# Kernel optimization log

Measured on AMD Instinct MI355X. Metric: run time of the kernel, lower is better.

Reference implementation:

```python
import jax, jax.numpy as jnp
import numpy as np
import math

B_CAPS, C_CAPS, K, P, STRIDE, ITERS = 32, 32, 3, 4, 2, 3
PSIZE = P * P
EPS = 1e-8
LAMBDA = 1e-3
LN_2PI = math.log(2.0 * math.pi)


def setup_inputs() -> dict:
    key = jax.random.key(0)
    k1, k2 = jax.random.split(key)
    # input: (b, h, w, B*(P*P+1)); activations must be non-negative (sigmoid-range)
    x = jax.random.uniform(k1, (4, 16, 16, B_CAPS * (PSIZE + 1)), dtype=jnp.float32)
    # nn.Parameter(torch.randn(1, K*K*B, P, P))
    weights = jax.random.normal(k2, (1, K * K * B_CAPS, P, P), dtype=jnp.float32)
    beta_u = jnp.zeros((C_CAPS,), jnp.float32)
    beta_a = jnp.zeros((C_CAPS,), jnp.float32)
    return {"x": x, "weights": weights, "beta_u": beta_u, "beta_a": beta_a}


def _add_patches(x):
    # torch add_pathes: zero-pad 1 on each side, gather KxK patches with stride
    b, h, w, c = x.shape
    x = jnp.pad(x, ((0, 0), (1, 1), (1, 1), (0, 0)))
    hp = h + 2
    oh = (hp - K) // STRIDE + 1
    idxs = np.arange(0, hp - K + 1, STRIDE)[:, None] + np.arange(K)[None, :]  # (oh, K)
    x = x[:, idxs, :, :]        # (b, oh, K, hp, c)
    x = x[:, :, :, idxs, :]     # (b, oh, K, ow, K, c)
    x = jnp.transpose(x, (0, 1, 3, 2, 4, 5))  # (b, oh, ow, K, K, c)
    return x, oh, oh


def _m_step(a_in, r, v, beta_u, beta_a):
    # a_in: (n, Bk, 1), r: (n, Bk, C), v: (n, Bk, C, psize)
    n = v.shape[0]
    r = r * a_in
    r = r / (jnp.sum(r, axis=2, keepdims=True) + EPS)
    r_sum = jnp.sum(r, axis=1, keepdims=True)              # (n, 1, C)
    coeff = (r / (r_sum + EPS))[..., None]                 # (n, Bk, C, 1)
    mu = jnp.sum(coeff * v, axis=1, keepdims=True)         # (n, 1, C, psize)
    sigma_sq = jnp.sum(coeff * (v - mu) ** 2, axis=1, keepdims=True) + EPS
    # cost_h: (n, C, psize)
    cost_h = (beta_u[:, None] + jnp.log(jnp.sqrt(sigma_sq[:, 0]))) * jnp.transpose(r_sum, (0, 2, 1))
    a_out = jax.nn.sigmoid(LAMBDA * (beta_a - jnp.sum(cost_h, axis=2)))  # (n, C)
    return a_out, mu, sigma_sq


def _e_step(mu, sigma_sq, a_out, v):
    ln_p = -(v - mu) ** 2 / (2.0 * sigma_sq) - jnp.log(jnp.sqrt(sigma_sq)) - 0.5 * LN_2PI
    ln_ap = jnp.sum(ln_p, axis=3) + jnp.log(a_out)[:, None, :]  # (n, Bk, C)
    return jax.nn.softmax(ln_ap, axis=2)


def _em_routing(v, a_in, beta_u, beta_a):
    n, Bk, C, _ = v.shape
    r = jnp.full((n, Bk, C), 1.0 / C, dtype=v.dtype)
    mu = a_out = None
    for it in range(ITERS):
        a_out, mu, sigma_sq = _m_step(a_in, r, v, beta_u, beta_a)
        if it < ITERS - 1:
            r = _e_step(mu, sigma_sq, a_out, v)
    return mu, a_out


def reference(x, weights, beta_u, beta_a):
    b = x.shape[0]
    patches, oh, ow = _add_patches(x)                       # (b, oh, ow, K, K, B*(psize+1))
    n = b * oh * ow
    Bk = K * K * B_CAPS
    p_in = patches[..., : B_CAPS * PSIZE].reshape(n, Bk, P, P)
    a_in = patches[..., B_CAPS * PSIZE :].reshape(n, Bk, 1)
    # votes: pose_i @ W_i (weights have no C axis in this repo -> shared across out-caps)
    v = jnp.einsum("nipq,iqr->nipr", p_in, weights[0]).reshape(n, Bk, 1, PSIZE)
    v = jnp.broadcast_to(v, (n, Bk, C_CAPS, PSIZE))
    mu, a_out = _em_routing(v, a_in, beta_u, beta_a)
    p_out = mu.reshape(b, oh, ow, C_CAPS * PSIZE)
    a_out = a_out.reshape(b, oh, ow, C_CAPS)
    return jnp.concatenate([p_out, a_out], axis=-1)        # (b, oh, ow, C*(psize+1))
```

## Files before the change

### kernel.cpp

```cpp
#include <hip/hip_runtime.h>
#include <math.h>

#define NTH 1024

typedef unsigned uint2v __attribute__((ext_vector_type(2)));

template <int CTRL>
__device__ __forceinline__ float dpp_mov(float x) {
  return __int_as_float(__builtin_amdgcn_mov_dpp(__float_as_int(x), CTRL, 0xF, 0xF, true));
}
__device__ __forceinline__ float row_sum16(float x) {
  x += dpp_mov<0x128>(x);
  x += dpp_mov<0x124>(x);
  x += dpp_mov<0x122>(x);
  x += dpp_mov<0x121>(x);
  return x;
}
__device__ __forceinline__ float row_max16(float x) {
  x = fmaxf(x, dpp_mov<0x128>(x));
  x = fmaxf(x, dpp_mov<0x124>(x));
  x = fmaxf(x, dpp_mov<0x122>(x));
  x = fmaxf(x, dpp_mov<0x121>(x));
  return x;
}
__device__ __forceinline__ float sum32(float x) {
  x = row_sum16(x);
  uint2v p = __builtin_amdgcn_permlane16_swap(__float_as_uint(x), __float_as_uint(x), false, false);
  return __uint_as_float(p.x) + __uint_as_float(p.y);
}
__device__ __forceinline__ float max32(float x) {
  x = row_max16(x);
  uint2v p = __builtin_amdgcn_permlane16_swap(__float_as_uint(x), __float_as_uint(x), false, false);
  return fmaxf(__uint_as_float(p.x), __uint_as_float(p.y));
}
__device__ __forceinline__ float sum_halves(float x) {
  uint2v p = __builtin_amdgcn_permlane32_swap(__float_as_uint(x), __float_as_uint(x), false, false);
  return __uint_as_float(p.x) + __uint_as_float(p.y);
}

__device__ __forceinline__ int swz8(int q, int c) { return (q + c) & 7; }

__launch_bounds__(NTH, 4)
__global__ void convcaps_em_kernel(const float* __restrict__ x,
                                   const float* __restrict__ wts,
                                   const float* __restrict__ beta_u,
                                   const float* __restrict__ beta_a,
                                   float* __restrict__ out) {
  constexpr int BK = 288;
  constexpr float EPS = 1e-8f;
  constexpr float LAM = 1e-3f;

  __shared__ __align__(16) float v_lds[BK * 16];
  __shared__ float w_lds[BK];
  __shared__ __align__(8) float part_lds[32 * 32];
  __shared__ float rsum_lds[32];
  __shared__ __align__(16) float stage_lds[16 * 1024];
  __shared__ __align__(16) float muinv2_lds[32 * 32];
  __shared__ float lnac_lds[32];
  __shared__ float mu0_lds[16], i2s0_lds[16], sc0_lds[2];

  const int t = threadIdx.x;
  const int n = blockIdx.x;
  const int b  = n >> 6;
  const int oy = (n >> 3) & 7;
  const int ox = n & 7;

  if (t < BK) {
    const int kk = t >> 5, cap = t & 31;
    const int kh = kk / 3, kw = kk - kh * 3;
    const int iy = oy * 2 - 1 + kh, ix = ox * 2 - 1 + kw;
    float val = 0.0f;
    if ((unsigned)iy < 16u && (unsigned)ix < 16u)
      val = x[(((b * 16 + iy) * 16) + ix) * 544 + 512 + cap];
    w_lds[t] = val / (val + EPS);
  }
  for (int task = t; task < BK * 4; task += NTH) {
    const int i = task >> 2, p = task & 3;
    const int kk = i >> 5, cap = i & 31;
    const int kh = kk / 3, kw = kk - kh * 3;
    const int iy = oy * 2 - 1 + kh, ix = ox * 2 - 1 + kw;
    float4 vv = make_float4(0.f, 0.f, 0.f, 0.f);
    if ((unsigned)iy < 16u && (unsigned)ix < 16u) {
      const float* px = x + ((((b * 16 + iy) * 16) + ix) * 544 + cap * 16 + p * 4);
      const float4 pin = *reinterpret_cast<const float4*>(px);
      const float* pw = wts + i * 16;
      const float4 w0 = *reinterpret_cast<const float4*>(pw + 0);
      const float4 w1 = *reinterpret_cast<const float4*>(pw + 4);
      const float4 w2 = *reinterpret_cast<const float4*>(pw + 8);
      const float4 w3 = *reinterpret_cast<const float4*>(pw + 12);
      vv.x = pin.x * w0.x + pin.y * w1.x + pin.z * w2.x + pin.w * w3.x;
      vv.y = pin.x * w0.y + pin.y * w1.y + pin.z * w2.y + pin.w * w3.y;
      vv.z = pin.x * w0.z + pin.y * w1.z + pin.z * w2.z + pin.w * w3.z;
      vv.w = pin.x * w0.w + pin.y * w1.w + pin.z * w2.w + pin.w * w3.w;
    }
    *reinterpret_cast<float4*>(&v_lds[i * 16 + p * 4]) = vv;
  }
  __syncthreads();

  const int c32 = t & 31;
  const int g32 = t >> 5;
  const int wv  = t >> 6;
  const int ln  = t & 63;
  const int cS  = (t >> 4) & 31;
  const int pS  = t & 15;
  const float bu = beta_u[cS];
  const float ba = beta_a[cS];

  if (t < 512) {
    const int h = t >> 4;
    float aw = 0.f, a1 = 0.f, a2 = 0.f;
    #pragma unroll
    for (int k = 0; k < 9; ++k) {
      const int i = h * 9 + k;
      const float wvv = w_lds[i];
      const float vv = v_lds[i * 16 + pS];
      aw += wvv;
      a1 = fmaf(wvv, vv, a1);
      a2 = fmaf(wvv * vv, vv, a2);
    }
    *reinterpret_cast<float2*>(&part_lds[(h * 16 + pS) * 2]) = make_float2(a1, a2);
    if (pS == 0) rsum_lds[h] = aw;
  }
  __syncthreads();
  if (t < 16) {
    float m0 = 0.f, a1 = 0.f, a2 = 0.f;
    #pragma unroll
    for (int h = 0; h < 32; ++h) {
      m0 += rsum_lds[h];
      const float2 f2 = *reinterpret_cast<const float2*>(&part_lds[(h * 16 + t) * 2]);
      a1 += f2.x; a2 += f2.y;
    }
    const float D0 = m0 + 32.f * EPS;
    const float mu = a1 / D0;
    float sig = (a2 - mu * (2.f * a1 - mu * m0)) / D0;
    sig = fmaxf(sig, 0.f) + EPS;
    const float ls = row_sum16(0.5f * __logf(sig));
    mu0_lds[t] = mu;
    i2s0_lds[t] = 0.5f / sig;
    if (t == 0) { sc0_lds[0] = m0 * 0.03125f; sc0_lds[1] = ls; }
  }
  __syncthreads();
  if (t < 512) {
    *reinterpret_cast<float2*>(
        &muinv2_lds[cS * 32 + (swz8(pS >> 1, cS) << 2) + ((pS & 1) << 1)]) =
        make_float2(mu0_lds[pS], i2s0_lds[pS]);
    if (pS == 0) {
      const float rs0 = sc0_lds[0], ls = sc0_lds[1];
      const float z = LAM * (ba - rs0 * (16.f * bu + ls));
      lnac_lds[cS] = -__logf(1.f + __expf(-z)) - ls;
    }
  }
  __syncthreads();

  for (int it = 0; it < 2; ++it) {
    {
      float muc[16], isc[16];
      #pragma unroll
      for (int q = 0; q < 8; ++q) {
        const float4 f =
            *reinterpret_cast<const float4*>(&muinv2_lds[c32 * 32 + (swz8(q, c32) << 2)]);
        muc[2 * q] = f.x; isc[2 * q] = f.y;
        muc[2 * q + 1] = f.z; isc[2 * q + 1] = f.w;
      }
      const float lna = lnac_lds[c32];
      const float lmax = max32(lna);
      float s1[16], s2[16];
      #pragma unroll
      for (int p2 = 0; p2 < 16; ++p2) { s1[p2] = 0.f; s2[p2] = 0.f; }
      float colsum = 0.f;
      #pragma unroll 3
      for (int pass = 0; pass < 9; ++pass) {
        const int i = pass * 32 + g32;
        const float4 v0 = *reinterpret_cast<const float4*>(&v_lds[i * 16 + 0]);
        const float4 v1 = *reinterpret_cast<const float4*>(&v_lds[i * 16 + 4]);
        const float4 v2 = *reinterpret_cast<const float4*>(&v_lds[i * 16 + 8]);
        const float4 v3 = *reinterpret_cast<const float4*>(&v_lds[i * 16 + 12]);
        float a0 = 0.f, a1 = 0.f, a2 = 0.f, a3 = 0.f, d;
        d = v0.x - muc[0];  a0 = fmaf(d * d, isc[0],  a0);
        d = v0.y - muc[1];  a1 = fmaf(d * d, isc[1],  a1);
        d = v0.z - muc[2];  a2 = fmaf(d * d, isc[2],  a2);
        d = v0.w - muc[3];  a3 = fmaf(d * d, isc[3],  a3);
        d = v1.x - muc[4];  a0 = fmaf(d * d, isc[4],  a0);
        d = v1.y - muc[5];  a1 = fmaf(d * d, isc[5],  a1);
        d = v1.z - muc[6];  a2 = fmaf(d * d, isc[6],  a2);
        d = v1.w - muc[7];  a3 = fmaf(d * d, isc[7],  a3);
        d = v2.x - muc[8];  a0 = fmaf(d * d, isc[8],  a0);
        d = v2.y - muc[9];  a1 = fmaf(d * d, isc[9],  a1);
        d = v2.z - muc[10]; a2 = fmaf(d * d, isc[10], a2);
        d = v2.w - muc[11]; a3 = fmaf(d * d, isc[11], a3);
        d = v3.x - muc[12]; a0 = fmaf(d * d, isc[12], a0);
        d = v3.y - muc[13]; a1 = fmaf(d * d, isc[13], a1);
        d = v3.z - muc[14]; a2 = fmaf(d * d, isc[14], a2);
        d = v3.w - muc[15]; a3 = fmaf(d * d, isc[15], a3);
        const float lnap = lna - ((a0 + a1) + (a2 + a3));
        const float e = __expf(lnap - lmax);
        const float ss = sum32(e);
        const float rn = e * (w_lds[i] * __builtin_amdgcn_rcpf(ss + 1e-30f));
        colsum += rn;
        float tv;
        tv = rn * v0.x; s1[0]  += tv; s2[0]  = fmaf(tv, v0.x, s2[0]);
        tv = rn * v0.y; s1[1]  += tv; s2[1]  = fmaf(tv, v0.y, s2[1]);
        tv = rn * v0.z; s1[2]  += tv; s2[2]  = fmaf(tv, v0.z, s2[2]);
        tv = rn * v0.w; s1[3]  += tv; s2[3]  = fmaf(tv, v0.w, s2[3]);
        tv = rn * v1.x; s1[4]  += tv; s2[4]  = fmaf(tv, v1.x, s2[4]);
        tv = rn * v1.y; s1[5]  += tv; s2[5]  = fmaf(tv, v1.y, s2[5]);
        tv = rn * v1.z; s1[6]  += tv; s2[6]  = fmaf(tv, v1.z, s2[6]);
        tv = rn * v1.w; s1[7]  += tv; s2[7]  = fmaf(tv, v1.w, s2[7]);
        tv = rn * v2.x; s1[8]  += tv; s2[8]  = fmaf(tv, v2.x, s2[8]);
        tv = rn * v2.y; s1[9]  += tv; s2[9]  = fmaf(tv, v2.y, s2[9]);
        tv = rn * v2.z; s1[10] += tv; s2[10] = fmaf(tv, v2.z, s2[10]);
        tv = rn * v2.w; s1[11] += tv; s2[11] = fmaf(tv, v2.w, s2[11]);
        tv = rn * v3.x; s1[12] += tv; s2[12] = fmaf(tv, v3.x, s2[12]);
        tv = rn * v3.y; s1[13] += tv; s2[13] = fmaf(tv, v3.y, s2[13]);
        tv = rn * v3.z; s1[14] += tv; s2[14] = fmaf(tv, v3.z, s2[14]);
        tv = rn * v3.w; s1[15] += tv; s2[15] = fmaf(tv, v3.w, s2[15]);
      }
      part_lds[g32 * 32 + c32] = colsum;
      #pragma unroll
      for (int p2 = 0; p2 < 16; ++p2) {
        s1[p2] = sum_halves(s1[p2]);
        s2[p2] = sum_halves(s2[p2]);
      }
      float* srow = &stage_lds[wv * 1024 + c32 * 32];
      if (ln < 32) {
        *reinterpret_cast<float4*>(&srow[swz8(0, c32) << 2]) = make_float4(s1[0], s1[1], s1[2], s1[3]);
        *reinterpret_cast<float4*>(&srow[swz8(1, c32) << 2]) = make_float4(s1[4], s1[5], s1[6], s1[7]);
        *reinterpret_cast<float4*>(&srow[swz8(2, c32) << 2]) = make_float4(s1[8], s1[9], s1[10], s1[11]);
        *reinterpret_cast<float4*>(&srow[swz8(3, c32) << 2]) = make_float4(s1[12], s1[13], s1[14], s1[15]);
      } else {
        *reinterpret_cast<float4*>(&srow[swz8(4, c32) << 2]) = make_float4(s2[0], s2[1], s2[2], s2[3]);
        *reinterpret_cast<float4*>(&srow[swz8(5, c32) << 2]) = make_float4(s2[4], s2[5], s2[6], s2[7]);
        *reinterpret_cast<float4*>(&srow[swz8(6, c32) << 2]) = make_float4(s2[8], s2[9], s2[10], s2[11]);
        *reinterpret_cast<float4*>(&srow[swz8(7, c32) << 2]) = make_float4(s2[12], s2[13], s2[14], s2[15]);
      }
    }
    __syncthreads();

    float gs1 = 0.f, gs2 = 0.f;
    if (t < 512) {
      const int off1 = cS * 32 + (swz8(pS >> 2, cS) << 2) + (pS & 3);
      const int off2 = cS * 32 + (swz8((pS >> 2) + 4, cS) << 2) + (pS & 3);
      #pragma unroll
      for (int w2 = 0; w2 < 16; ++w2) {
        gs1 += stage_lds[w2 * 1024 + off1];
        gs2 += stage_lds[w2 * 1024 + off2];
      }
    } else if (t < 544) {
      const int c = t - 512;
      float s = 0.f;
      #pragma unroll
      for (int g = 0; g < 32; ++g) s += part_lds[g * 32 + c];
      rsum_lds[c] = s;
    }
    __syncthreads();

    if (t < 512) {
      const float rs = rsum_lds[cS];
      const float D = rs + EPS;
      const float mu = gs1 / D;
      float sig = (gs2 - mu * (2.f * gs1 - mu * rs)) / D;
      sig = fmaxf(sig, 0.f) + EPS;
      const float lsum = row_sum16(0.5f * __logf(sig));
      const float z = LAM * (ba - rs * (16.f * bu + lsum));
      if (it == 0) {
        *reinterpret_cast<float2*>(
            &muinv2_lds[cS * 32 + (swz8(pS >> 1, cS) << 2) + ((pS & 1) << 1)]) =
            make_float2(mu, 0.5f / sig);
        if (pS == 0) lnac_lds[cS] = -__logf(1.f + __expf(-z)) - lsum;
      } else {
        out[n * 544 + t] = mu;
        if (pS == 0) out[n * 544 + 512 + cS] = 1.f / (1.f + __expf(-z));
      }
    }
    __syncthreads();
  }
}

extern "C" void kernel_launch(void* const* d_in, const int* in_sizes, int n_in,
                              void* d_out, int out_size, void* d_ws, size_t ws_size,
                              hipStream_t stream) {
  const float* x   = (const float*)d_in[0];
  const float* wts = (const float*)d_in[1];
  const float* bu  = (const float*)d_in[2];
  const float* ba  = (const float*)d_in[3];
  float* out = (float*)d_out;
  hipLaunchKernelGGL(convcaps_em_kernel, dim3(256), dim3(NTH), 0, stream,
                     x, wts, bu, ba, out);
}
```

Baseline: 80.60 us.

## Pack routing math into float2 vectors, use per-row softmax max, drop a barrier

Changes the mu/inv-sigma LDS layout so pairs of elements sit next to each other, then rewrites the E-step distance and the weighted sums as two-wide float vectors. The goal is to let the compiler emit packed FP32 instructions (v_pk_fma/v_pk_mul) and roughly halve the VALU instruction count in the hot loop. The softmax max is now taken over each row's lnap instead of a shared lna max, which adds a max32 reduction per pass but is numerically safer. The column-sum reduction is done redundantly by every one of the 512 threads, which removes one __syncthreads at the cost of extra LDS reads.

```diff
diff --git a/kernel.cpp b/kernel.cpp
--- a/kernel.cpp
+++ b/kernel.cpp
@@ -4,6 +4,8 @@
 #define NTH 1024
 
 typedef unsigned uint2v __attribute__((ext_vector_type(2)));
+typedef float f32x2 __attribute__((ext_vector_type(2)));
+typedef float f32x4 __attribute__((ext_vector_type(4)));
 
 template <int CTRL>
 __device__ __forceinline__ float dpp_mov(float x) {
@@ -36,6 +38,12 @@
 __device__ __forceinline__ float sum_halves(float x) {
   uint2v p = __builtin_amdgcn_permlane32_swap(__float_as_uint(x), __float_as_uint(x), false, false);
   return __uint_as_float(p.x) + __uint_as_float(p.y);
+}
+__device__ __forceinline__ f32x2 sum_halves2(f32x2 v) {
+  f32x2 r;
+  r.x = sum_halves(v.x);
+  r.y = sum_halves(v.y);
+  return r;
 }
 
 __device__ __forceinline__ int swz8(int q, int c) { return (q + c) & 7; }
@@ -141,9 +149,9 @@
   }
   __syncthreads();
   if (t < 512) {
-    *reinterpret_cast<float2*>(
-        &muinv2_lds[cS * 32 + (swz8(pS >> 1, cS) << 2) + ((pS & 1) << 1)]) =
-        make_float2(mu0_lds[pS], i2s0_lds[pS]);
+    const int base = cS * 32 + (swz8(pS >> 1, cS) << 2);
+    muinv2_lds[base + (pS & 1)] = mu0_lds[pS];
+    muinv2_lds[base + 2 + (pS & 1)] = i2s0_lds[pS];
     if (pS == 0) {
       const float rs0 = sc0_lds[0], ls = sc0_lds[1];
       const float z = LAM * (ba - rs0 * (16.f * bu + ls));
@@ -154,90 +162,91 @@
 
   for (int it = 0; it < 2; ++it) {
     {
-      float muc[16], isc[16];
+      f32x2 mu2[8], is2[8];
       #pragma unroll
       for (int q = 0; q < 8; ++q) {
-        const float4 f =
-            *reinterpret_cast<const float4*>(&muinv2_lds[c32 * 32 + (swz8(q, c32) << 2)]);
-        muc[2 * q] = f.x; isc[2 * q] = f.y;
-        muc[2 * q + 1] = f.z; isc[2 * q + 1] = f.w;
+        const f32x4 f =
+            *reinterpret_cast<const f32x4*>(&muinv2_lds[c32 * 32 + (swz8(q, c32) << 2)]);
+        mu2[q] = f.xy;
+        is2[q] = f.zw;
       }
       const float lna = lnac_lds[c32];
-      const float lmax = max32(lna);
-      float s1[16], s2[16];
-      #pragma unroll
-      for (int p2 = 0; p2 < 16; ++p2) { s1[p2] = 0.f; s2[p2] = 0.f; }
+      f32x2 s1v[8], s2v[8];
+      #pragma unroll
+      for (int q = 0; q < 8; ++q) {
+        s1v[q] = f32x2{0.f, 0.f};
+        s2v[q] = f32x2{0.f, 0.f};
+      }
       float colsum = 0.f;
       #pragma unroll 3
       for (int pass = 0; pass < 9; ++pass) {
         const int i = pass * 32 + g32;
-        const float4 v0 = *reinterpret_cast<const float4*>(&v_lds[i * 16 + 0]);
-        const float4 v1 = *reinterpret_cast<const float4*>(&v_lds[i * 16 + 4]);
-        const float4 v2 = *reinterpret_cast<const float4*>(&v_lds[i * 16 + 8]);
-        const float4 v3 = *reinterpret_cast<const float4*>(&v_lds[i * 16 + 12]);
-        float a0 = 0.f, a1 = 0.f, a2 = 0.f, a3 = 0.f, d;
-        d = v0.x - muc[0];  a0 = fmaf(d * d, isc[0],  a0);
-        d = v0.y - muc[1];  a1 = fmaf(d * d, isc[1],  a1);
-        d = v0.z - muc[2];  a2 = fmaf(d * d, isc[2],  a2);
-        d = v0.w - muc[3];  a3 = fmaf(d * d, isc[3],  a3);
-        d = v1.x - muc[4];  a0 = fmaf(d * d, isc[4],  a0);
-        d = v1.y - muc[5];  a1 = fmaf(d * d, isc[5],  a1);
-        d = v1.z - muc[6];  a2 = fmaf(d * d, isc[6],  a2);
-        d = v1.w - muc[7];  a3 = fmaf(d * d, isc[7],  a3);
-        d = v2.x - muc[8];  a0 = fmaf(d * d, isc[8],  a0);
-        d = v2.y - muc[9];  a1 = fmaf(d * d, isc[9],  a1);
-        d = v2.z - muc[10]; a2 = fmaf(d * d, isc[10], a2);
-        d = v2.w - muc[11]; a3 = fmaf(d * d, isc[11], a3);
-        d = v3.x - muc[12]; a0 = fmaf(d * d, isc[12], a0);
-        d = v3.y - muc[13]; a1 = fmaf(d * d, isc[13], a1);
-        d = v3.z - muc[14]; a2 = fmaf(d * d, isc[14], a2);
-        d = v3.w - muc[15]; a3 = fmaf(d * d, isc[15], a3);
-        const float lnap = lna - ((a0 + a1) + (a2 + a3));
-        const float e = __expf(lnap - lmax);
+        const f32x4 q0 = *reinterpret_cast<const f32x4*>(&v_lds[i * 16 + 0]);
+        const f32x4 q1 = *reinterpret_cast<const f32x4*>(&v_lds[i * 16 + 4]);
+        const f32x4 q2 = *reinterpret_cast<const f32x4*>(&v_lds[i * 16 + 8]);
+        const f32x4 q3 = *reinterpret_cast<const f32x4*>(&v_lds[i * 16 + 12]);
+        f32x2 aa = f32x2{0.f, 0.f}, ab = f32x2{0.f, 0.f}, d;
+        d = q0.xy - mu2[0]; aa = __builtin_elementwise_fma(d * d, is2[0], aa);
+        d = q0.zw - mu2[1]; ab = __builtin_elementwise_fma(d * d, is2[1], ab);
+        d = q1.xy - mu2[2]; aa = __builtin_elementwise_fma(d * d, is2[2], aa);
+        d = q1.zw - mu2[3]; ab = __builtin_elementwise_fma(d * d, is2[3], ab);
+        d = q2.xy - mu2[4]; aa = __builtin_elementwise_fma(d * d, is2[4], aa);
+        d = q2.zw - mu2[5]; ab = __builtin_elementwise_fma(d * d, is2[5], ab);
+        d = q3.xy - mu2[6]; aa = __builtin_elementwise_fma(d * d, is2[6], aa);
+        d = q3.zw - mu2[7]; ab = __builtin_elementwise_fma(d * d, is2[7], ab);
+        const f32x2 at = aa + ab;
+        const float lnap = lna - (at.x + at.y);
+        const float mx = max32(lnap);
+        const float e = __expf(lnap - mx);
         const float ss = sum32(e);
         const float rn = e * (w_lds[i] * __builtin_amdgcn_rcpf(ss + 1e-30f));
         colsum += rn;
-        float tv;
-        tv = rn * v0.x; s1[0]  += tv; s2[0]  = fmaf(tv, v0.x, s2[0]);
-        tv = rn * v0.y; s1[1]  += tv; s2[1]  = fmaf(tv, v0.y, s2[1]);
-        tv = rn * v0.z; s1[2]  += tv; s2[2]  = fmaf(tv, v0.z, s2[2]);
-        tv = rn * v0.w; s1[3]  += tv; s2[3]  = fmaf(tv, v0.w, s2[3]);
-        tv = rn * v1.x; s1[4]  += tv; s2[4]  = fmaf(tv, v1.x, s2[4]);
-        tv = rn * v1.y; s1[5]  += tv; s2[5]  = fmaf(tv, v1.y, s2[5]);
-        tv = rn * v1.z; s1[6]  += tv; s2[6]  = fmaf(tv, v1.z, s2[6]);
-        tv = rn * v1.w; s1[7]  += tv; s2[7]  = fmaf(tv, v1.w, s2[7]);
-        tv = rn * v2.x; s1[8]  += tv; s2[8]  = fmaf(tv, v2.x, s2[8]);
-        tv = rn * v2.y; s1[9]  += tv; s2[9]  = fmaf(tv, v2.y, s2[9]);
-        tv = rn * v2.z; s1[10] += tv; s2[10] = fmaf(tv, v2.z, s2[10]);
-        tv = rn * v2.w; s1[11] += tv; s2[11] = fmaf(tv, v2.w, s2[11]);
-        tv = rn * v3.x; s1[12] += tv; s2[12] = fmaf(tv, v3.x, s2[12]);
-        tv = rn * v3.y; s1[13] += tv; s2[13] = fmaf(tv, v3.y, s2[13]);
-        tv = rn * v3.z; s1[14] += tv; s2[14] = fmaf(tv, v3.z, s2[14]);
-        tv = rn * v3.w; s1[15] += tv; s2[15] = fmaf(tv, v3.w, s2[15]);
+        f32x2 tv;
+        tv = q0.xy * rn; s1v[0] += tv; s2v[0] = __builtin_elementwise_fma(tv, q0.xy, s2v[0]);
+        tv = q0.zw * rn; s1v[1] += tv; s2v[1] = __builtin_elementwise_fma(tv, q0.zw, s2v[1]);
+        tv = q1.xy * rn; s1v[2] += tv; s2v[2] = __builtin_elementwise_fma(tv, q1.xy, s2v[2]);
+        tv = q1.zw * rn; s1v[3] += tv; s2v[3] = __builtin_elementwise_fma(tv, q1.zw, s2v[3]);
+        tv = q2.xy * rn; s1v[4] += tv; s2v[4] = __builtin_elementwise_fma(tv, q2.xy, s2v[4]);
+        tv = q2.zw * rn; s1v[5] += tv; s2v[5] = __builtin_elementwise_fma(tv, q2.zw, s2v[5]);
+        tv = q3.xy * rn; s1v[6] += tv; s2v[6] = __builtin_elementwise_fma(tv, q3.xy, s2v[6]);
+        tv = q3.zw * rn; s1v[7] += tv; s2v[7] = __builtin_elementwise_fma(tv, q3.zw, s2v[7]);
       }
       part_lds[g32 * 32 + c32] = colsum;
       #pragma unroll
-      for (int p2 = 0; p2 < 16; ++p2) {
-        s1[p2] = sum_halves(s1[p2]);
-        s2[p2] = sum_halves(s2[p2]);
+      for (int q = 0; q < 8; ++q) {
+        s1v[q] = sum_halves2(s1v[q]);
+        s2v[q] = sum_halves2(s2v[q]);
       }
       float* srow = &stage_lds[wv * 1024 + c32 * 32];
       if (ln < 32) {
-        *reinterpret_cast<float4*>(&srow[swz8(0, c32) << 2]) = make_float4(s1[0], s1[1], s1[2], s1[3]);
-        *reinterpret_cast<float4*>(&srow[swz8(1, c32) << 2]) = make_float4(s1[4], s1[5], s1[6], s1[7]);
-        *reinterpret_cast<float4*>(&srow[swz8(2, c32) << 2]) = make_float4(s1[8], s1[9], s1[10], s1[11]);
-        *reinterpret_cast<float4*>(&srow[swz8(3, c32) << 2]) = make_float4(s1[12], s1[13], s1[14], s1[15]);
+        f32x4 o;
+        o.xy = s1v[0]; o.zw = s1v[1];
+        *reinterpret_cast<f32x4*>(&srow[swz8(0, c32) << 2]) = o;
+        o.xy = s1v[2]; o.zw = s1v[3];
+        *reinterpret_cast<f32x4*>(&srow[swz8(1, c32) << 2]) = o;
+        o.xy = s1v[4]; o.zw = s1v[5];
+        *reinterpret_cast<f32x4*>(&srow[swz8(2, c32) << 2]) = o;
+        o.xy = s1v[6]; o.zw = s1v[7];
+        *reinterpret_cast<f32x4*>(&srow[swz8(3, c32) << 2]) = o;
       } else {
-        *reinterpret_cast<float4*>(&srow[swz8(4, c32) << 2]) = make_float4(s2[0], s2[1], s2[2], s2[3]);
-        *reinterpret_cast<float4*>(&srow[swz8(5, c32) << 2]) = make_float4(s2[4], s2[5], s2[6], s2[7]);
-        *reinterpret_cast<float4*>(&srow[swz8(6, c32) << 2]) = make_float4(s2[8], s2[9], s2[10], s2[11]);
-        *reinterpret_cast<float4*>(&srow[swz8(7, c32) << 2]) = make_float4(s2[12], s2[13], s2[14], s2[15]);
+        f32x4 o;
+        o.xy = s2v[0]; o.zw = s2v[1];
+        *reinterpret_cast<f32x4*>(&srow[swz8(4, c32) << 2]) = o;
+        o.xy = s2v[2]; o.zw = s2v[3];
+        *reinterpret_cast<f32x4*>(&srow[swz8(5, c32) << 2]) = o;
+        o.xy = s2v[4]; o.zw = s2v[5];
+        *reinterpret_cast<f32x4*>(&srow[swz8(6, c32) << 2]) = o;
+        o.xy = s2v[6]; o.zw = s2v[7];
+        *reinterpret_cast<f32x4*>(&srow[swz8(7, c32) << 2]) = o;
       }
     }
     __syncthreads();
 
-    float gs1 = 0.f, gs2 = 0.f;
     if (t < 512) {
+      float rs = 0.f;
+      #pragma unroll
+      for (int g = 0; g < 32; ++g) rs += part_lds[g * 32 + cS];
+      float gs1 = 0.f, gs2 = 0.f;
       const int off1 = cS * 32 + (swz8(pS >> 2, cS) << 2) + (pS & 3);
       const int off2 = cS * 32 + (swz8((pS >> 2) + 4, cS) << 2) + (pS & 3);
       #pragma unroll
@@ -245,17 +254,6 @@
         gs1 += stage_lds[w2 * 1024 + off1];
         gs2 += stage_lds[w2 * 1024 + off2];
       }
-    } else if (t < 544) {
-      const int c = t - 512;
-      float s = 0.f;
-      #pragma unroll
-      for (int g = 0; g < 32; ++g) s += part_lds[g * 32 + c];
-      rsum_lds[c] = s;
-    }
-    __syncthreads();
-
-    if (t < 512) {
-      const float rs = rsum_lds[cS];
       const float D = rs + EPS;
       const float mu = gs1 / D;
       float sig = (gs2 - mu * (2.f * gs1 - mu * rs)) / D;
@@ -263,9 +261,9 @@
       const float lsum = row_sum16(0.5f * __logf(sig));
       const float z = LAM * (ba - rs * (16.f * bu + lsum));
       if (it == 0) {
-        *reinterpret_cast<float2*>(
-            &muinv2_lds[cS * 32 + (swz8(pS >> 1, cS) << 2) + ((pS & 1) << 1)]) =
-            make_float2(mu, 0.5f / sig);
+        const int base = cS * 32 + (swz8(pS >> 1, cS) << 2);
+        muinv2_lds[base + (pS & 1)] = mu;
+        muinv2_lds[base + 2 + (pS & 1)] = 0.5f / sig;
         if (pS == 0) lnac_lds[cS] = -__logf(1.f + __expf(-z)) - lsum;
       } else {
         out[n * 544 + t] = mu;
```

Result: no change. 79.83 us (-1.0%).
